# Kernel optimization log

Measured on AMD Instinct MI355X. Metric: run time of the kernel, lower is better.

## Reference

```python
import jax, jax.numpy as jnp
import numpy as np

IN_DIM, OUT_DIM, EDGE_DIM = 64, 64, 16
B, N = 16384, 33  # N = K+1, K=32 neighbors
EPS = 1e-5


def setup_inputs() -> dict:
    key = jax.random.key(0)
    ks = jax.random.split(key, 10)
    s_in = 1.0 / np.sqrt(IN_DIM)
    s_e = 1.0 / np.sqrt(EDGE_DIM)
    s_a = 1.0 / np.sqrt(3 * OUT_DIM)
    return {
        "nodes": jax.random.normal(ks[0], (B, N, IN_DIM), jnp.float32),
        "edge_features": jax.random.normal(ks[1], (B, N - 1, EDGE_DIM), jnp.float32),
        "W_w": jax.random.uniform(ks[2], (IN_DIM, OUT_DIM), jnp.float32, -s_in, s_in),
        "W_b": jax.random.uniform(ks[3], (OUT_DIM,), jnp.float32, -s_in, s_in),
        "We_w": jax.random.uniform(ks[4], (EDGE_DIM, OUT_DIM), jnp.float32, -s_e, s_e),
        "We_b": jax.random.uniform(ks[5], (OUT_DIM,), jnp.float32, -s_e, s_e),
        "attn_w": jax.random.uniform(ks[6], (3 * OUT_DIM, 1), jnp.float32, -s_a, s_a),
        "attn_b": jax.random.uniform(ks[7], (1,), jnp.float32, -s_a, s_a),
        "gamma": jnp.ones((OUT_DIM,), jnp.float32),
        "beta": jnp.zeros((OUT_DIM,), jnp.float32),
    }


def _layer_norm(x, gamma, beta):
    mu = jnp.mean(x, axis=-1, keepdims=True)
    var = jnp.mean(jnp.square(x - mu), axis=-1, keepdims=True)
    return (x - mu) * jax.lax.rsqrt(var + EPS) * gamma + beta


def reference(nodes, edge_features, W_w, W_b, We_w, We_b, attn_w, attn_b, gamma, beta):
    # h: (B, N, out_dim)
    h = jnp.einsum("bni,io->bno", nodes, W_w) + W_b
    target = h[:, 0:1, :]                     # (B, 1, D)
    neighbors = h[:, 1:, :]                   # (B, K, D)
    edge_h = jnp.einsum("bke,eo->bko", edge_features, We_w) + We_b  # (B, K, D)
    K = neighbors.shape[1]
    attn_input = jnp.concatenate(
        [jnp.broadcast_to(target, (h.shape[0], K, h.shape[2])), neighbors, edge_h],
        axis=-1,
    )  # (B, K, 3D)
    scores = jnp.einsum("bkf,fo->bko", attn_input, attn_w) + attn_b  # (B, K, 1)
    attn = jax.nn.softmax(scores, axis=1)     # softmax over neighbor dim
    messages = jnp.sum(neighbors * attn, axis=1, keepdims=True)  # (B, 1, D)
    h_new = jnp.concatenate([target + messages, neighbors], axis=1)  # (B, N, D)
    return _layer_norm(h_new, gamma, beta)
```

## Files before the change

### kernel.cpp

```cpp
#include <hip/hip_runtime.h>
#include <math.h>

#define NN 33
#define KK 32
#define D  64
#define ED 16
#define EPSV 1e-5f

#define FOR16(M) M(0) M(1) M(2) M(3) M(4) M(5) M(6) M(7) \
                 M(8) M(9) M(10) M(11) M(12) M(13) M(14) M(15)

#define W_DECL(q) float4 Wc##q;
#define W_LOAD(q) Wc##q = make_float4(W_w[(4*(q)+0)*D + lane], \
                                      W_w[(4*(q)+1)*D + lane], \
                                      W_w[(4*(q)+2)*D + lane], \
                                      W_w[(4*(q)+3)*D + lane]);
#define W_FMA(q) { const float4 xv = xr[(q)];            \
                   acc = fmaf(xv.x, Wc##q.x, acc);       \
                   acc = fmaf(xv.y, Wc##q.y, acc);       \
                   acc = fmaf(xv.z, Wc##q.z, acc);       \
                   acc = fmaf(xv.w, Wc##q.w, acc); }

__global__
__attribute__((amdgpu_flat_work_group_size(256, 256), amdgpu_waves_per_eu(2, 4)))
void gat_kernel(const float* __restrict__ nodes,
                const float* __restrict__ edges,
                const float* __restrict__ W_w,
                const float* __restrict__ W_b,
                const float* __restrict__ We_w,
                const float* __restrict__ We_b,
                const float* __restrict__ attn_w,
                const float* __restrict__ attn_b,
                const float* __restrict__ gamma,
                const float* __restrict__ beta,
                float* __restrict__ out,
                int B)
{
    __shared__ float s_aw[192];
    __shared__ float s_v2[ED];
    __shared__ float s_scores[KK];
    __shared__ float s_attn[KK];
    __shared__ float s_part[4 * D];
    __shared__ float s_tdot;
    __shared__ float s_const;

    const int tid  = threadIdx.x;
    const int wave = tid >> 6;
    const int lane = tid & 63;

    FOR16(W_DECL)
    FOR16(W_LOAD)

    const float r_wb    = W_b[lane];
    const float r_gamma = gamma[lane];
    const float r_beta  = beta[lane];
    const float aw0_l   = attn_w[lane];
    const float aw1_l   = attn_w[D + lane];

    if (tid < 192) s_aw[tid] = attn_w[tid];
    __syncthreads();
    if (tid < ED) {
        float v = 0.f;
        #pragma unroll
        for (int o = 0; o < D; ++o) v = fmaf(We_w[tid * D + o], s_aw[128 + o], v);
        s_v2[tid] = v;
    } else if (tid == ED) {
        float c = attn_b[0];
        #pragma unroll
        for (int o = 0; o < D; ++o) c = fmaf(We_b[o], s_aw[128 + o], c);
        s_const = c;
    }
    __syncthreads();

    for (int b = blockIdx.x; b < B; b += gridDim.x) {
        const float* xb = nodes + (size_t)b * (NN * D);

        float h[9];
        #pragma unroll
        for (int j = 0; j < 9; ++j) {
            const int n = wave + 4 * j;
            if (n < NN) {
                const float4* xr = (const float4*)(xb + n * D);
                float acc = r_wb;
                FOR16(W_FMA)
                h[j] = acc;
            }
        }

        #pragma unroll
        for (int j = 0; j < 9; ++j) {
            const int n = wave + 4 * j;
            if (n < NN) {
                float p = h[j] * (n == 0 ? aw0_l : aw1_l);
                #pragma unroll
                for (int s = 1; s < 64; s <<= 1) p += __shfl_xor(p, s, 64);
                if (lane == 0) {
                    if (n == 0) s_tdot = p; else s_scores[n - 1] = p;
                }
            }
        }
        __syncthreads();

        if (wave == 0 && lane < KK) {
            const float4* eg = (const float4*)(edges + ((size_t)b * KK + lane) * ED);
            float edot = 0.f;
            #pragma unroll
            for (int q = 0; q < ED / 4; ++q) {
                const float4 e = eg[q];
                edot = fmaf(e.x, s_v2[4*q+0], edot);
                edot = fmaf(e.y, s_v2[4*q+1], edot);
                edot = fmaf(e.z, s_v2[4*q+2], edot);
                edot = fmaf(e.w, s_v2[4*q+3], edot);
            }
            const float sk = s_scores[lane] + s_tdot + edot + s_const;
            float m = sk;
            #pragma unroll
            for (int s = 1; s < 32; s <<= 1) m = fmaxf(m, __shfl_xor(m, s, 64));
            const float ex = __expf(sk - m);
            float sum = ex;
            #pragma unroll
            for (int s = 1; s < 32; s <<= 1) sum += __shfl_xor(sum, s, 64);
            s_attn[lane] = ex / sum;
        }
        __syncthreads();

        float part = 0.f;
        #pragma unroll
        for (int j = 0; j < 9; ++j) {
            const int n = wave + 4 * j;
            if (n >= 1 && n < NN) part = fmaf(s_attn[n - 1], h[j], part);
        }
        s_part[wave * D + lane] = part;
        __syncthreads();

        if (wave == 0) {
            h[0] += s_part[lane] + s_part[D + lane] + s_part[2 * D + lane] + s_part[3 * D + lane];
        }

        #pragma unroll
        for (int j = 0; j < 9; ++j) {
            const int n = wave + 4 * j;
            if (n < NN) {
                const float x = h[j];
                float s1 = x, s2 = x * x;
                #pragma unroll
                for (int s = 1; s < 64; s <<= 1) {
                    s1 += __shfl_xor(s1, s, 64);
                    s2 += __shfl_xor(s2, s, 64);
                }
                const float mu  = s1 * (1.f / 64.f);
                const float var = s2 * (1.f / 64.f) - mu * mu;
                const float r   = rsqrtf(var + EPSV);
                out[((size_t)b * NN + n) * D + lane] = (x - mu) * r * r_gamma + r_beta;
            }
        }
    }
}

extern "C" void kernel_launch(void* const* d_in, const int* in_sizes, int n_in,
                              void* d_out, int out_size, void* d_ws, size_t ws_size,
                              hipStream_t stream)
{
    const float* nodes  = (const float*)d_in[0];
    const float* edges  = (const float*)d_in[1];
    const float* W_w    = (const float*)d_in[2];
    const float* W_b    = (const float*)d_in[3];
    const float* We_w   = (const float*)d_in[4];
    const float* We_b   = (const float*)d_in[5];
    const float* attn_w = (const float*)d_in[6];
    const float* attn_b = (const float*)d_in[7];
    const float* gamma  = (const float*)d_in[8];
    const float* beta   = (const float*)d_in[9];
    float* out = (float*)d_out;

    const int B = in_sizes[0] / (NN * D);

    dim3 grid(2048), block(256);
    gat_kernel<<<grid, block, 0, stream>>>(nodes, edges, W_w, W_b, We_w, We_b,
                                           attn_w, attn_b, gamma, beta, out, B);
}
```

Measured before the change: 821.9 us.

## Split edge-dot into separate kernel and process one batch per wave without barriers

Moves the edge-feature dot product (with the attention constant folded in) into a separate pre-kernel that writes per-edge scores to workspace. The main kernel now assigns one batch element per wave, keeping all 33 node rows in registers. Softmax, message aggregation and layer norm run entirely with wave shuffles, so the shared memory and __syncthreads between phases are gone. The trade-offs are higher register pressure (33-entry h array plus 64 weight registers, waves_per_eu lowered), an extra kernel launch, and a workspace round trip.

New measurement: 825.4 us. Within noise of the previous version (+0.4%).

```diff
diff --git a/kernel.cpp b/kernel.cpp
--- a/kernel.cpp
+++ b/kernel.cpp
@@ -15,35 +15,58 @@
                                       W_w[(4*(q)+1)*D + lane], \
                                       W_w[(4*(q)+2)*D + lane], \
                                       W_w[(4*(q)+3)*D + lane]);
-#define W_FMA(q) { const float4 xv = xr[(q)];            \
+#define W_FMA(q) { const float4 xv = xrow[(q)];          \
                    acc = fmaf(xv.x, Wc##q.x, acc);       \
                    acc = fmaf(xv.y, Wc##q.y, acc);       \
                    acc = fmaf(xv.z, Wc##q.z, acc);       \
                    acc = fmaf(xv.w, Wc##q.w, acc); }
 
+__global__ __launch_bounds__(256)
+void edot_kernel(const float* __restrict__ edges,
+                 const float* __restrict__ We_w,
+                 const float* __restrict__ We_b,
+                 const float* __restrict__ attn_w,
+                 const float* __restrict__ attn_b,
+                 float* __restrict__ edot, int nk)
+{
+    __shared__ float s_v2[ED];
+    __shared__ float s_c;
+    const int tid = threadIdx.x;
+    if (tid < ED) {
+        float v = 0.f;
+        #pragma unroll
+        for (int o = 0; o < D; ++o) v = fmaf(We_w[tid * D + o], attn_w[2 * D + o], v);
+        s_v2[tid] = v;
+    } else if (tid == ED) {
+        float c = attn_b[0];
+        #pragma unroll
+        for (int o = 0; o < D; ++o) c = fmaf(We_b[o], attn_w[2 * D + o], c);
+        s_c = c;
+    }
+    __syncthreads();
+    const int gid = blockIdx.x * 256 + tid;
+    const int k = gid >> 2, e = gid & 3;
+    if (k < nk) {
+        const float4 ev = ((const float4*)edges)[(size_t)k * 4 + e];
+        float p = ev.x * s_v2[4*e+0] + ev.y * s_v2[4*e+1]
+                + ev.z * s_v2[4*e+2] + ev.w * s_v2[4*e+3];
+        p += __shfl_xor(p, 1, 64);
+        p += __shfl_xor(p, 2, 64);
+        if (e == 0) edot[k] = p + s_c;
+    }
+}
+
 __global__
-__attribute__((amdgpu_flat_work_group_size(256, 256), amdgpu_waves_per_eu(2, 4)))
-void gat_kernel(const float* __restrict__ nodes,
-                const float* __restrict__ edges,
-                const float* __restrict__ W_w,
-                const float* __restrict__ W_b,
-                const float* __restrict__ We_w,
-                const float* __restrict__ We_b,
-                const float* __restrict__ attn_w,
-                const float* __restrict__ attn_b,
-                const float* __restrict__ gamma,
-                const float* __restrict__ beta,
-                float* __restrict__ out,
-                int B)
+__attribute__((amdgpu_flat_work_group_size(256, 256), amdgpu_waves_per_eu(1, 3)))
+void gat_main(const float* __restrict__ nodes,
+              const float* __restrict__ W_w,
+              const float* __restrict__ W_b,
+              const float* __restrict__ attn_w,
+              const float* __restrict__ gamma,
+              const float* __restrict__ beta,
+              const float* __restrict__ edot,
+              float* __restrict__ out, int B)
 {
-    __shared__ float s_aw[192];
-    __shared__ float s_v2[ED];
-    __shared__ float s_scores[KK];
-    __shared__ float s_attn[KK];
-    __shared__ float s_part[4 * D];
-    __shared__ float s_tdot;
-    __shared__ float s_const;
-
     const int tid  = threadIdx.x;
     const int wave = tid >> 6;
     const int lane = tid & 63;
@@ -54,105 +77,59 @@
     const float r_wb    = W_b[lane];
     const float r_gamma = gamma[lane];
     const float r_beta  = beta[lane];
-    const float aw0_l   = attn_w[lane];
-    const float aw1_l   = attn_w[D + lane];
+    const float aw0     = attn_w[lane];
+    const float aw1     = attn_w[D + lane];
 
-    if (tid < 192) s_aw[tid] = attn_w[tid];
-    __syncthreads();
-    if (tid < ED) {
-        float v = 0.f;
+    const int stride = gridDim.x * 4;
+    for (int b = blockIdx.x * 4 + wave; b < B; b += stride) {
+        const float4* __restrict__ xr = (const float4*)(nodes + (size_t)b * (NN * D));
+
+        float h[NN];
+        float sc = 0.f, tdot = 0.f;
         #pragma unroll
-        for (int o = 0; o < D; ++o) v = fmaf(We_w[tid * D + o], s_aw[128 + o], v);
-        s_v2[tid] = v;
-    } else if (tid == ED) {
-        float c = attn_b[0];
-        #pragma unroll
-        for (int o = 0; o < D; ++o) c = fmaf(We_b[o], s_aw[128 + o], c);
-        s_const = c;
-    }
-    __syncthreads();
-
-    for (int b = blockIdx.x; b < B; b += gridDim.x) {
-        const float* xb = nodes + (size_t)b * (NN * D);
-
-        float h[9];
-        #pragma unroll
-        for (int j = 0; j < 9; ++j) {
-            const int n = wave + 4 * j;
-            if (n < NN) {
-                const float4* xr = (const float4*)(xb + n * D);
-                float acc = r_wb;
-                FOR16(W_FMA)
-                h[j] = acc;
-            }
+        for (int n = 0; n < NN; ++n) {
+            const float4* xrow = xr + n * 16;
+            float acc = r_wb;
+            FOR16(W_FMA)
+            h[n] = acc;
+            float p = acc * (n == 0 ? aw0 : aw1);
+            #pragma unroll
+            for (int s = 1; s < 64; s <<= 1) p += __shfl_xor(p, s, 64);
+            if (n == 0) tdot = p;
+            else        sc = (lane == n - 1) ? p : sc;
         }
 
+        const float ed = edot[(size_t)b * KK + (lane & 31)];
+        const float sk = sc + tdot + ed;
+        float m = sk;
         #pragma unroll
-        for (int j = 0; j < 9; ++j) {
-            const int n = wave + 4 * j;
-            if (n < NN) {
-                float p = h[j] * (n == 0 ? aw0_l : aw1_l);
-                #pragma unroll
-                for (int s = 1; s < 64; s <<= 1) p += __shfl_xor(p, s, 64);
-                if (lane == 0) {
-                    if (n == 0) s_tdot = p; else s_scores[n - 1] = p;
-                }
+        for (int s = 1; s < 32; s <<= 1) m = fmaxf(m, __shfl_xor(m, s, 64));
+        const float ex = __expf(sk - m);
+        float sum = ex;
+        #pragma unroll
+        for (int s = 1; s < 32; s <<= 1) sum += __shfl_xor(sum, s, 64);
+        const float attn = ex / sum;
+
+        float msg = 0.f;
+        #pragma unroll
+        for (int k = 0; k < KK; ++k)
+            msg = fmaf(__shfl(attn, k, 64), h[k + 1], msg);
+        h[0] += msg;
+
+        float* __restrict__ orow = out + (size_t)b * (NN * D) + lane;
+        #pragma unroll
+        for (int n = 0; n < NN; ++n) {
+            const float x = h[n];
+            float s1 = x, s2 = x * x;
+            #pragma unroll
+            for (int s = 1; s < 64; s <<= 1) {
+                s1 += __shfl_xor(s1, s, 64);
+                s2 += __shfl_xor(s2, s, 64);
             }
-        }
-        __syncthreads();
-
-        if (wave == 0 && lane < KK) {
-            const float4* eg = (const float4*)(edges + ((size_t)b * KK + lane) * ED);
-            float edot = 0.f;
-            #pragma unroll
-            for (int q = 0; q < ED / 4; ++q) {
-                const float4 e = eg[q];
-                edot = fmaf(e.x, s_v2[4*q+0], edot);
-                edot = fmaf(e.y, s_v2[4*q+1], edot);
-                edot = fmaf(e.z, s_v2[4*q+2], edot);
-                edot = fmaf(e.w, s_v2[4*q+3], edot);
-            }
-            const float sk = s_scores[lane] + s_tdot + edot + s_const;
-            float m = sk;
-            #pragma unroll
-            for (int s = 1; s < 32; s <<= 1) m = fmaxf(m, __shfl_xor(m, s, 64));
-            const float ex = __expf(sk - m);
-            float sum = ex;
-            #pragma unroll
-            for (int s = 1; s < 32; s <<= 1) sum += __shfl_xor(sum, s, 64);
-            s_attn[lane] = ex / sum;
-        }
-        __syncthreads();
-
-        float part = 0.f;
-        #pragma unroll
-        for (int j = 0; j < 9; ++j) {
-            const int n = wave + 4 * j;
-            if (n >= 1 && n < NN) part = fmaf(s_attn[n - 1], h[j], part);
-        }
-        s_part[wave * D + lane] = part;
-        __syncthreads();
-
-        if (wave == 0) {
-            h[0] += s_part[lane] + s_part[D + lane] + s_part[2 * D + lane] + s_part[3 * D + lane];
-        }
-
-        #pragma unroll
-        for (int j = 0; j < 9; ++j) {
-            const int n = wave + 4 * j;
-            if (n < NN) {
-                const float x = h[j];
-                float s1 = x, s2 = x * x;
-                #pragma unroll
-                for (int s = 1; s < 64; s <<= 1) {
-                    s1 += __shfl_xor(s1, s, 64);
-                    s2 += __shfl_xor(s2, s, 64);
-                }
-                const float mu  = s1 * (1.f / 64.f);
-                const float var = s2 * (1.f / 64.f) - mu * mu;
-                const float r   = rsqrtf(var + EPSV);
-                out[((size_t)b * NN + n) * D + lane] = (x - mu) * r * r_gamma + r_beta;
-            }
+            const float mu  = s1 * (1.f / 64.f);
+            const float var = s2 * (1.f / 64.f) - mu * mu;
+            const float r   = rsqrtf(var + EPSV);
+            orow[n * D] = (x - mu) * r * r_gamma + r_beta;
         }
     }
 }
@@ -171,11 +148,15 @@
     const float* attn_b = (const float*)d_in[7];
     const float* gamma  = (const float*)d_in[8];
     const float* beta   = (const float*)d_in[9];
-    float* out = (float*)d_out;
+    float* out  = (float*)d_out;
+    float* edot = (float*)d_ws;
 
-    const int B = in_sizes[0] / (NN * D);
+    const int B  = in_sizes[0] / (NN * D);
+    const int nk = B * KK;
 
-    dim3 grid(2048), block(256);
-    gat_kernel<<<grid, block, 0, stream>>>(nodes, edges, W_w, W_b, We_w, We_b,
-                                           attn_w, attn_b, gamma, beta, out, B);
+    edot_kernel<<<(nk * 4 + 255) / 256, 256, 0, stream>>>(
+        edges, We_w, We_b, attn_w, attn_b, edot, nk);
+
+    gat_main<<<1024, 256, 0, stream>>>(
+        nodes, W_w, W_b, attn_w, gamma, beta, edot, out, B);
 }
```
